# Kernel tuning notes

Measured on AMD Instinct MI355X. Metric: run time of the kernel, lower is better.

Reference implementation:

```python
import jax, jax.numpy as jnp
import numpy as np
import math

B, L, H, NH = 8, 200, 128, 2
HD = H // NH  # head dim = 64
TIME_VOCAB = 32
LN_EPS = 1e-12


def setup_inputs() -> dict:
    key = jax.random.key(0)
    ks = jax.random.split(key, 16)
    rn = lambda k, shape, s=0.02: (jax.random.normal(k, shape, jnp.float32) * s)
    return {
        "input_tensor": jax.random.normal(ks[0], (B, L, H), jnp.float32),
        "time_seq": jnp.sort(jax.random.randint(ks[1], (B, L), 0, 100000, jnp.int64), axis=-1),
        "attention_mask": jnp.zeros((B, 1, L, L), jnp.float32),
        "Wq": rn(ks[2], (H, H)), "bq": jnp.zeros((H,), jnp.float32),
        "Wk": rn(ks[3], (H, H)), "bk": jnp.zeros((H,), jnp.float32),
        "Wv": rn(ks[4], (H, H)), "bv": jnp.zeros((H,), jnp.float32),
        "Wd": rn(ks[5], (H, H)), "bd": jnp.zeros((H,), jnp.float32),
        "ln_g": jnp.ones((H,), jnp.float32), "ln_b": jnp.zeros((H,), jnp.float32),
        "key_time_table": rn(ks[6], (TIME_VOCAB, H)),
        "value_time_table": rn(ks[7], (TIME_VOCAB, H)),
        "key_pos_table": rn(ks[8], (L, H)),
        "value_pos_table": rn(ks[9], (L, H)),
    }


def _split_heads(x):
    # [B, L, H] -> [B, NH, L, HD]
    b, l, _ = x.shape
    return x.reshape(b, l, NH, HD).transpose(0, 2, 1, 3)


def reference(input_tensor, time_seq, attention_mask,
              Wq, bq, Wk, bk, Wv, bv, Wd, bd, ln_g, ln_b,
              key_time_table, value_time_table, key_pos_table, value_pos_table):
    b, l, h = input_tensor.shape

    # position embeddings (same for all batches)
    kpos = key_pos_table[:l].reshape(l, NH, HD).transpose(1, 0, 2)[None]    # [1,NH,L,HD]
    vpos = value_pos_table[:l].reshape(l, NH, HD).transpose(1, 0, 2)[None]  # [1,NH,L,HD]

    q = _split_heads(input_tensor @ Wq + bq)  # [B,NH,L,HD]
    k = _split_heads(input_tensor @ Wk + bk)
    v = _split_heads(input_tensor @ Wv + bv)

    scores = jnp.einsum('bhqd,bhkd->bhqk', q, k + kpos)

    # time decay: diff[b,i,j] = floor(log(1 + |t_i - t_j|))
    t = time_seq
    diff_idx = jnp.log1p(jnp.abs(t[:, :, None] - t[:, None, :]).astype(jnp.float32)).astype(jnp.int32)  # [B,L,L]

    # [B,L,L,H] -> [B,NH,L,L,HD]
    kt = key_time_table[diff_idx].reshape(b, l, l, NH, HD).transpose(0, 3, 1, 2, 4)
    vt = value_time_table[diff_idx].reshape(b, l, l, NH, HD).transpose(0, 3, 1, 2, 4)

    time_scores = jnp.einsum('bhqd,bhqkd->bhqk', q, kt)

    scores = (scores + time_scores) / math.sqrt(HD)
    scores = scores + attention_mask  # additive mask, broadcast over heads

    probs = jax.nn.softmax(scores, axis=-1)  # attn_dropout is identity in eval

    ctx = jnp.einsum('bhqk,bhkd->bhqd', probs, v + vpos)
    # NOTE: original uses raw (masked, pre-softmax) attention_scores here
    time_ctx = jnp.einsum('bhqk,bhqkd->bhqd', scores, vt)
    ctx = ctx + time_ctx

    ctx = ctx.transpose(0, 2, 1, 3).reshape(b, l, h)  # merge heads
    hidden = ctx @ Wd + bd                            # out_dropout identity in eval

    x = hidden + input_tensor
    mu = x.mean(-1, keepdims=True)
    var = ((x - mu) ** 2).mean(-1, keepdims=True)
    return (x - mu) / jnp.sqrt(var + LN_EPS) * ln_g + ln_b
```

## Files before the change

kernel.cpp:

```cpp
#include <hip/hip_runtime.h>
#include <math.h>

#define B_ 8
#define L_ 200
#define H_ 128
#define NH_ 2
#define HD_ 64
#define LP_ 256
#define TV_ 32
#define RQ_ 8
#define TQ_ 2

__global__ __launch_bounds__(128)
void qkv_kernel(const float* __restrict__ X,
                const float* __restrict__ Wq, const float* __restrict__ bq,
                const float* __restrict__ Wk, const float* __restrict__ bk,
                const float* __restrict__ Wv, const float* __restrict__ bv,
                const float* __restrict__ kpt, const float* __restrict__ vpt,
                float* __restrict__ Q, float* __restrict__ Kt, float* __restrict__ Vp){
    const int r0 = blockIdx.x * RQ_;
    const int m  = blockIdx.y;
    const int j  = threadIdx.x;
    __shared__ float xs[RQ_][H_];
    #pragma unroll
    for (int r = 0; r < RQ_; ++r) xs[r][j] = X[(r0 + r) * H_ + j];
    __syncthreads();
    const float* W = (m == 0) ? Wq : ((m == 1) ? Wk : Wv);
    float acc[RQ_];
    #pragma unroll
    for (int r = 0; r < RQ_; ++r) acc[r] = 0.f;
    #pragma unroll 8
    for (int i = 0; i < H_; ++i) {
        const float w = W[i * H_ + j];
        #pragma unroll
        for (int r = 0; r < RQ_; ++r) acc[r] += xs[r][i] * w;
    }
    const int h = j >> 6, d = j & 63;
    if (m == 0) {
        const float bj = bq[j];
        #pragma unroll
        for (int r = 0; r < RQ_; ++r) Q[(r0 + r) * H_ + j] = acc[r] + bj;
    } else if (m == 1) {
        const float bj = bk[j];
        #pragma unroll
        for (int r = 0; r < RQ_; ++r) {
            const int row = r0 + r, b = row / L_, l = row % L_;
            Kt[((b * NH_ + h) * HD_ + d) * LP_ + l] = acc[r] + bj + kpt[l * H_ + j];
        }
    } else {
        const float bj = bv[j];
        #pragma unroll
        for (int r = 0; r < RQ_; ++r) {
            const int row = r0 + r, b = row / L_, l = row % L_;
            Vp[((b * NH_ + h) * L_ + l) * HD_ + d] = acc[r] + bj + vpt[l * H_ + j];
        }
    }
}

__global__ __launch_bounds__(256)
void attn_out_kernel(const float* __restrict__ Q, const float* __restrict__ Kt,
                     const float* __restrict__ Vp, const int* __restrict__ tseq,
                     const float* __restrict__ mask,
                     const float* __restrict__ ktt, const float* __restrict__ vtt,
                     const float* __restrict__ Wd, const float* __restrict__ bd,
                     const float* __restrict__ X, const float* __restrict__ g,
                     const float* __restrict__ bb, float* __restrict__ out){
    const int b  = blockIdx.x / (L_ / TQ_);
    const int q0 = (blockIdx.x % (L_ / TQ_)) * TQ_;
    const int w  = threadIdx.x >> 6, lane = threadIdx.x & 63;
    const int h  = w & 1, qr = w >> 1, q = q0 + qr;
    const int bh = b * NH_ + h;

    __shared__ float ktt_s[TV_][H_ + 1];
    __shared__ float vtt_s[TV_][H_ + 1];
    __shared__ __align__(16) float qs [4][HD_];
    __shared__ float qkt[4][TV_];
    __shared__ float ss [4][TV_];
    __shared__ __align__(16) float ps [4][LP_];
    __shared__ float ctx_s[TQ_][H_];
    __shared__ float red1[4], red2[4];

    for (int t = threadIdx.x; t < TV_ * H_; t += 256) {
        ktt_s[t >> 7][t & 127] = ktt[t];
        vtt_s[t >> 7][t & 127] = vtt[t];
    }
    qs[w][lane] = Q[(b * L_ + q) * H_ + h * HD_ + lane];
    if (lane < TV_) ss[w][lane] = 0.f;
    __syncthreads();

    {
        const int i = lane & 31, half = lane >> 5;
        float a = 0.f;
        #pragma unroll 8
        for (int d = 0; d < 32; ++d)
            a += qs[w][half * 32 + d] * ktt_s[i][h * HD_ + half * 32 + d];
        a += __shfl_xor(a, 32);
        if (lane < TV_) qkt[w][lane] = a;
    }

    const float4* kt4 = (const float4*)(Kt + (size_t)bh * HD_ * LP_);
    float4 sA = make_float4(0.f, 0.f, 0.f, 0.f);
    float4 sB = make_float4(0.f, 0.f, 0.f, 0.f);
    #pragma unroll 8
    for (int d = 0; d < HD_; d += 2) {
        const float q0d = qs[w][d], q1d = qs[w][d + 1];
        const float4 k0 = kt4[d * (LP_ / 4) + lane];
        const float4 k1 = kt4[(d + 1) * (LP_ / 4) + lane];
        sA.x += q0d * k0.x; sA.y += q0d * k0.y; sA.z += q0d * k0.z; sA.w += q0d * k0.w;
        sB.x += q1d * k1.x; sB.y += q1d * k1.y; sB.z += q1d * k1.z; sB.w += q1d * k1.w;
    }
    float sv[4] = {sA.x + sB.x, sA.y + sB.y, sA.z + sB.z, sA.w + sB.w};
    const int k0i = lane * 4;
    float mx = -INFINITY;
    if (k0i < L_) {
        const float4 m4 = ((const float4*)(mask + ((size_t)(b * L_ + q)) * L_))[lane];
        const int4   t4 = ((const int4*)(tseq + b * L_))[lane];
        const int    tq = tseq[b * L_ + q];
        const float mv[4] = {m4.x, m4.y, m4.z, m4.w};
        const int   tk[4] = {t4.x, t4.y, t4.z, t4.w};
        #pragma unroll
        for (int jj = 0; jj < 4; ++jj) {
            int dt = tq - tk[jj]; if (dt < 0) dt = -dt;
            int idx = (int)log1pf((float)dt);
            if (idx > TV_ - 1) idx = TV_ - 1;
            float s = (sv[jj] + qkt[w][idx]) * 0.125f + mv[jj];
            sv[jj] = s;
            atomicAdd(&ss[w][idx], s);
            if (s > mx) mx = s;
        }
    } else {
        sv[0] = sv[1] = sv[2] = sv[3] = -INFINITY;
    }
    for (int off = 32; off; off >>= 1) { float o = __shfl_xor(mx, off); if (o > mx) mx = o; }
    float sum = 0.f, ev[4];
    #pragma unroll
    for (int jj = 0; jj < 4; ++jj) {
        float e = (k0i + jj < L_) ? __expf(sv[jj] - mx) : 0.f;
        ev[jj] = e; sum += e;
    }
    for (int off = 32; off; off >>= 1) sum += __shfl_xor(sum, off);
    ((float4*)ps[w])[lane] = make_float4(ev[0], ev[1], ev[2], ev[3]);

    const float inv = 1.f / sum;
    const float* vp = Vp + (size_t)bh * L_ * HD_;
    float c = 0.f;
    #pragma unroll 8
    for (int k = 0; k < L_; ++k) c += ps[w][k] * vp[k * HD_ + lane];
    c *= inv;
    float tc = 0.f;
    #pragma unroll 8
    for (int i = 0; i < TV_; ++i) tc += ss[w][i] * vtt_s[i][h * HD_ + lane];
    ctx_s[qr][h * HD_ + lane] = c + tc;
    __syncthreads();

    const int r = threadIdx.x >> 7, j = threadIdx.x & 127;
    float acc = 0.f;
    #pragma unroll 8
    for (int i = 0; i < H_; ++i) acc += ctx_s[r][i] * Wd[i * H_ + j];
    const int row = b * L_ + q0 + r;
    const float x = acc + bd[j] + X[row * H_ + j];

    float s = x;
    for (int off = 32; off; off >>= 1) s += __shfl_xor(s, off);
    if (lane == 0) red1[w] = s;
    __syncthreads();
    const float mean = (red1[2 * r] + red1[2 * r + 1]) * (1.f / H_);
    const float dx = x - mean;
    float s2 = dx * dx;
    for (int off = 32; off; off >>= 1) s2 += __shfl_xor(s2, off);
    if (lane == 0) red2[w] = s2;
    __syncthreads();
    const float var = (red2[2 * r] + red2[2 * r + 1]) * (1.f / H_);
    const float y = dx * rsqrtf(var + 1e-12f) * g[j] + bb[j];
    out[row * H_ + j] = y;
}

extern "C" void kernel_launch(void* const* d_in, const int* in_sizes, int n_in,
                              void* d_out, int out_size, void* d_ws, size_t ws_size,
                              hipStream_t stream) {
    const float* X    = (const float*)d_in[0];
    const int*   tseq = (const int*)  d_in[1];
    const float* mask = (const float*)d_in[2];
    const float* Wq = (const float*)d_in[3],  *bq = (const float*)d_in[4];
    const float* Wk = (const float*)d_in[5],  *bk = (const float*)d_in[6];
    const float* Wv = (const float*)d_in[7],  *bv = (const float*)d_in[8];
    const float* Wd = (const float*)d_in[9],  *bd = (const float*)d_in[10];
    const float* g  = (const float*)d_in[11], *bb = (const float*)d_in[12];
    const float* ktt = (const float*)d_in[13], *vtt = (const float*)d_in[14];
    const float* kpt = (const float*)d_in[15], *vpt = (const float*)d_in[16];

    float* ws  = (float*)d_ws;
    float* Q   = ws;
    float* Kt  = Q   + B_ * L_ * H_;
    float* Vp  = Kt  + B_ * NH_ * HD_ * LP_;

    dim3 g1(B_ * L_ / RQ_, 3);
    qkv_kernel<<<g1, 128, 0, stream>>>(X, Wq, bq, Wk, bk, Wv, bv, kpt, vpt, Q, Kt, Vp);
    attn_out_kernel<<<B_ * (L_ / TQ_), 256, 0, stream>>>(Q, Kt, Vp, tseq, mask, ktt, vtt,
                                                         Wd, bd, X, g, bb, (float*)d_out);
}
```

Before: 121.2 us.

## Process two query rows per wavefront to share K/V/Wd loads

Each block now covers four query rows, with each wavefront computing scores, softmax, context and output projection for two rows at once. Every K, V, time-table and Wd value loaded is reused for both rows, and the per-block shared-memory table setup is amortised over twice as many rows. In exchange the grid halves and register pressure rises, which may reduce latency hiding.

```diff
diff --git a/kernel.cpp b/kernel.cpp
--- a/kernel.cpp
+++ b/kernel.cpp
@@ -9,7 +9,6 @@
 #define LP_ 256
 #define TV_ 32
 #define RQ_ 8
-#define TQ_ 2
 
 __global__ __launch_bounds__(128)
 void qkv_kernel(const float* __restrict__ X,
@@ -65,114 +64,167 @@
                      const float* __restrict__ Wd, const float* __restrict__ bd,
                      const float* __restrict__ X, const float* __restrict__ g,
                      const float* __restrict__ bb, float* __restrict__ out){
-    const int b  = blockIdx.x / (L_ / TQ_);
-    const int q0 = (blockIdx.x % (L_ / TQ_)) * TQ_;
+    const int b  = blockIdx.x / (L_ / 4);
+    const int q0 = (blockIdx.x % (L_ / 4)) * 4;
     const int w  = threadIdx.x >> 6, lane = threadIdx.x & 63;
-    const int h  = w & 1, qr = w >> 1, q = q0 + qr;
+    const int h  = w & 1, qp = w >> 1;
+    const int qa = q0 + 2 * qp, qb = qa + 1;
     const int bh = b * NH_ + h;
 
     __shared__ float ktt_s[TV_][H_ + 1];
     __shared__ float vtt_s[TV_][H_ + 1];
-    __shared__ __align__(16) float qs [4][HD_];
-    __shared__ float qkt[4][TV_];
-    __shared__ float ss [4][TV_];
-    __shared__ __align__(16) float ps [4][LP_];
-    __shared__ float ctx_s[TQ_][H_];
-    __shared__ float red1[4], red2[4];
+    __shared__ __align__(16) float qs [4][2][HD_];
+    __shared__ __align__(16) float qkt[4][2][TV_];
+    __shared__ __align__(16) float ss [4][2][TV_];
+    __shared__ __align__(16) float ps [4][2][LP_];
+    __shared__ __align__(16) float ctx_s[4][H_];
+    __shared__ float redA[4], redB[4], red2A[4], red2B[4];
 
     for (int t = threadIdx.x; t < TV_ * H_; t += 256) {
         ktt_s[t >> 7][t & 127] = ktt[t];
         vtt_s[t >> 7][t & 127] = vtt[t];
     }
-    qs[w][lane] = Q[(b * L_ + q) * H_ + h * HD_ + lane];
-    if (lane < TV_) ss[w][lane] = 0.f;
+    qs[w][0][lane] = Q[(b * L_ + qa) * H_ + h * HD_ + lane];
+    qs[w][1][lane] = Q[(b * L_ + qb) * H_ + h * HD_ + lane];
+    ss[w][lane >> 5][lane & 31] = 0.f;
     __syncthreads();
 
     {
-        const int i = lane & 31, half = lane >> 5;
+        const int i = lane & 31, qsel = lane >> 5;
         float a = 0.f;
         #pragma unroll 8
-        for (int d = 0; d < 32; ++d)
-            a += qs[w][half * 32 + d] * ktt_s[i][h * HD_ + half * 32 + d];
-        a += __shfl_xor(a, 32);
-        if (lane < TV_) qkt[w][lane] = a;
+        for (int d = 0; d < HD_; ++d)
+            a += qs[w][qsel][d] * ktt_s[i][h * HD_ + d];
+        qkt[w][qsel][i] = a;
     }
 
     const float4* kt4 = (const float4*)(Kt + (size_t)bh * HD_ * LP_);
-    float4 sA = make_float4(0.f, 0.f, 0.f, 0.f);
-    float4 sB = make_float4(0.f, 0.f, 0.f, 0.f);
+    float4 sa = make_float4(0.f, 0.f, 0.f, 0.f);
+    float4 sb = make_float4(0.f, 0.f, 0.f, 0.f);
     #pragma unroll 8
-    for (int d = 0; d < HD_; d += 2) {
-        const float q0d = qs[w][d], q1d = qs[w][d + 1];
-        const float4 k0 = kt4[d * (LP_ / 4) + lane];
-        const float4 k1 = kt4[(d + 1) * (LP_ / 4) + lane];
-        sA.x += q0d * k0.x; sA.y += q0d * k0.y; sA.z += q0d * k0.z; sA.w += q0d * k0.w;
-        sB.x += q1d * k1.x; sB.y += q1d * k1.y; sB.z += q1d * k1.z; sB.w += q1d * k1.w;
-    }
-    float sv[4] = {sA.x + sB.x, sA.y + sB.y, sA.z + sB.z, sA.w + sB.w};
+    for (int d = 0; d < HD_; ++d) {
+        const float4 kv = kt4[d * (LP_ / 4) + lane];
+        const float qad = qs[w][0][d], qbd = qs[w][1][d];
+        sa.x += qad * kv.x; sa.y += qad * kv.y; sa.z += qad * kv.z; sa.w += qad * kv.w;
+        sb.x += qbd * kv.x; sb.y += qbd * kv.y; sb.z += qbd * kv.z; sb.w += qbd * kv.w;
+    }
+    float sva[4] = {sa.x, sa.y, sa.z, sa.w};
+    float svb[4] = {sb.x, sb.y, sb.z, sb.w};
     const int k0i = lane * 4;
-    float mx = -INFINITY;
+    float mxa = -INFINITY, mxb = -INFINITY;
     if (k0i < L_) {
-        const float4 m4 = ((const float4*)(mask + ((size_t)(b * L_ + q)) * L_))[lane];
-        const int4   t4 = ((const int4*)(tseq + b * L_))[lane];
-        const int    tq = tseq[b * L_ + q];
-        const float mv[4] = {m4.x, m4.y, m4.z, m4.w};
-        const int   tk[4] = {t4.x, t4.y, t4.z, t4.w};
+        const float4 m4a = ((const float4*)(mask + ((size_t)(b * L_ + qa)) * L_))[lane];
+        const float4 m4b = ((const float4*)(mask + ((size_t)(b * L_ + qb)) * L_))[lane];
+        const int4   t4  = ((const int4*)(tseq + b * L_))[lane];
+        const int    tqa = tseq[b * L_ + qa], tqb = tseq[b * L_ + qb];
+        const float mva[4] = {m4a.x, m4a.y, m4a.z, m4a.w};
+        const float mvb[4] = {m4b.x, m4b.y, m4b.z, m4b.w};
+        const int   tk[4]  = {t4.x, t4.y, t4.z, t4.w};
         #pragma unroll
         for (int jj = 0; jj < 4; ++jj) {
-            int dt = tq - tk[jj]; if (dt < 0) dt = -dt;
-            int idx = (int)log1pf((float)dt);
-            if (idx > TV_ - 1) idx = TV_ - 1;
-            float s = (sv[jj] + qkt[w][idx]) * 0.125f + mv[jj];
-            sv[jj] = s;
-            atomicAdd(&ss[w][idx], s);
-            if (s > mx) mx = s;
+            int dta = tqa - tk[jj]; if (dta < 0) dta = -dta;
+            int dtb = tqb - tk[jj]; if (dtb < 0) dtb = -dtb;
+            int ia = (int)log1pf((float)dta); if (ia > TV_ - 1) ia = TV_ - 1;
+            int ib = (int)log1pf((float)dtb); if (ib > TV_ - 1) ib = TV_ - 1;
+            float s_a = (sva[jj] + qkt[w][0][ia]) * 0.125f + mva[jj];
+            float s_b = (svb[jj] + qkt[w][1][ib]) * 0.125f + mvb[jj];
+            sva[jj] = s_a; svb[jj] = s_b;
+            atomicAdd(&ss[w][0][ia], s_a);
+            atomicAdd(&ss[w][1][ib], s_b);
+            if (s_a > mxa) mxa = s_a;
+            if (s_b > mxb) mxb = s_b;
         }
     } else {
-        sv[0] = sv[1] = sv[2] = sv[3] = -INFINITY;
-    }
-    for (int off = 32; off; off >>= 1) { float o = __shfl_xor(mx, off); if (o > mx) mx = o; }
-    float sum = 0.f, ev[4];
+        sva[0] = sva[1] = sva[2] = sva[3] = -INFINITY;
+        svb[0] = svb[1] = svb[2] = svb[3] = -INFINITY;
+    }
+    for (int off = 32; off; off >>= 1) {
+        float oa = __shfl_xor(mxa, off); if (oa > mxa) mxa = oa;
+        float ob = __shfl_xor(mxb, off); if (ob > mxb) mxb = ob;
+    }
+    float suma = 0.f, sumb = 0.f, eva[4], evb[4];
     #pragma unroll
     for (int jj = 0; jj < 4; ++jj) {
-        float e = (k0i + jj < L_) ? __expf(sv[jj] - mx) : 0.f;
-        ev[jj] = e; sum += e;
-    }
-    for (int off = 32; off; off >>= 1) sum += __shfl_xor(sum, off);
-    ((float4*)ps[w])[lane] = make_float4(ev[0], ev[1], ev[2], ev[3]);
-
-    const float inv = 1.f / sum;
+        float ea = (k0i + jj < L_) ? __expf(sva[jj] - mxa) : 0.f;
+        float eb = (k0i + jj < L_) ? __expf(svb[jj] - mxb) : 0.f;
+        eva[jj] = ea; suma += ea;
+        evb[jj] = eb; sumb += eb;
+    }
+    for (int off = 32; off; off >>= 1) { suma += __shfl_xor(suma, off); sumb += __shfl_xor(sumb, off); }
+    ((float4*)ps[w][0])[lane] = make_float4(eva[0], eva[1], eva[2], eva[3]);
+    ((float4*)ps[w][1])[lane] = make_float4(evb[0], evb[1], evb[2], evb[3]);
+
+    const float inva = 1.f / suma, invb = 1.f / sumb;
     const float* vp = Vp + (size_t)bh * L_ * HD_;
-    float c = 0.f;
+    const float4* psa4 = (const float4*)ps[w][0];
+    const float4* psb4 = (const float4*)ps[w][1];
+    float ca = 0.f, cb = 0.f;
+    #pragma unroll 5
+    for (int k4 = 0; k4 < L_ / 4; ++k4) {
+        const float4 pa = psa4[k4], pb = psb4[k4];
+        const int kb = k4 * 4;
+        const float v0 = vp[(kb + 0) * HD_ + lane];
+        const float v1 = vp[(kb + 1) * HD_ + lane];
+        const float v2 = vp[(kb + 2) * HD_ + lane];
+        const float v3 = vp[(kb + 3) * HD_ + lane];
+        ca += pa.x * v0; ca += pa.y * v1; ca += pa.z * v2; ca += pa.w * v3;
+        cb += pb.x * v0; cb += pb.y * v1; cb += pb.z * v2; cb += pb.w * v3;
+    }
+    ca *= inva; cb *= invb;
+    float tca = 0.f, tcb = 0.f;
+    const float4* ssa4 = (const float4*)ss[w][0];
+    const float4* ssb4 = (const float4*)ss[w][1];
+    #pragma unroll
+    for (int i4 = 0; i4 < TV_ / 4; ++i4) {
+        const float4 za = ssa4[i4], zb = ssb4[i4];
+        const int i = i4 * 4;
+        const float w0 = vtt_s[i + 0][h * HD_ + lane];
+        const float w1 = vtt_s[i + 1][h * HD_ + lane];
+        const float w2 = vtt_s[i + 2][h * HD_ + lane];
+        const float w3 = vtt_s[i + 3][h * HD_ + lane];
+        tca += za.x * w0; tca += za.y * w1; tca += za.z * w2; tca += za.w * w3;
+        tcb += zb.x * w0; tcb += zb.y * w1; tcb += zb.z * w2; tcb += zb.w * w3;
+    }
+    ctx_s[2 * qp + 0][h * HD_ + lane] = ca + tca;
+    ctx_s[2 * qp + 1][h * HD_ + lane] = cb + tcb;
+    __syncthreads();
+
+    const int r = threadIdx.x >> 7, j = threadIdx.x & 127;
+    const float4* ca4 = (const float4*)ctx_s[r];
+    const float4* cb4 = (const float4*)ctx_s[r + 2];
+    float acc_a = 0.f, acc_b = 0.f;
     #pragma unroll 8
-    for (int k = 0; k < L_; ++k) c += ps[w][k] * vp[k * HD_ + lane];
-    c *= inv;
-    float tc = 0.f;
-    #pragma unroll 8
-    for (int i = 0; i < TV_; ++i) tc += ss[w][i] * vtt_s[i][h * HD_ + lane];
-    ctx_s[qr][h * HD_ + lane] = c + tc;
-    __syncthreads();
-
-    const int r = threadIdx.x >> 7, j = threadIdx.x & 127;
-    float acc = 0.f;
-    #pragma unroll 8
-    for (int i = 0; i < H_; ++i) acc += ctx_s[r][i] * Wd[i * H_ + j];
-    const int row = b * L_ + q0 + r;
-    const float x = acc + bd[j] + X[row * H_ + j];
-
-    float s = x;
-    for (int off = 32; off; off >>= 1) s += __shfl_xor(s, off);
-    if (lane == 0) red1[w] = s;
-    __syncthreads();
-    const float mean = (red1[2 * r] + red1[2 * r + 1]) * (1.f / H_);
-    const float dx = x - mean;
-    float s2 = dx * dx;
-    for (int off = 32; off; off >>= 1) s2 += __shfl_xor(s2, off);
-    if (lane == 0) red2[w] = s2;
-    __syncthreads();
-    const float var = (red2[2 * r] + red2[2 * r + 1]) * (1.f / H_);
-    const float y = dx * rsqrtf(var + 1e-12f) * g[j] + bb[j];
-    out[row * H_ + j] = y;
+    for (int i4 = 0; i4 < H_ / 4; ++i4) {
+        const float4 xa = ca4[i4], xb = cb4[i4];
+        const int i = i4 * 4;
+        const float w0 = Wd[(i + 0) * H_ + j];
+        const float w1 = Wd[(i + 1) * H_ + j];
+        const float w2 = Wd[(i + 2) * H_ + j];
+        const float w3 = Wd[(i + 3) * H_ + j];
+        acc_a += xa.x * w0; acc_a += xa.y * w1; acc_a += xa.z * w2; acc_a += xa.w * w3;
+        acc_b += xb.x * w0; acc_b += xb.y * w1; acc_b += xb.z * w2; acc_b += xb.w * w3;
+    }
+    const int rowa = b * L_ + q0 + r, rowb = rowa + 2;
+    const float bdj = bd[j];
+    const float x_a = acc_a + bdj + X[rowa * H_ + j];
+    const float x_b = acc_b + bdj + X[rowb * H_ + j];
+
+    float s1a = x_a, s1b = x_b;
+    for (int off = 32; off; off >>= 1) { s1a += __shfl_xor(s1a, off); s1b += __shfl_xor(s1b, off); }
+    if (lane == 0) { redA[w] = s1a; redB[w] = s1b; }
+    __syncthreads();
+    const float meanA = (redA[2 * r] + redA[2 * r + 1]) * (1.f / H_);
+    const float meanB = (redB[2 * r] + redB[2 * r + 1]) * (1.f / H_);
+    const float dxa = x_a - meanA, dxb = x_b - meanB;
+    float s2a = dxa * dxa, s2b = dxb * dxb;
+    for (int off = 32; off; off >>= 1) { s2a += __shfl_xor(s2a, off); s2b += __shfl_xor(s2b, off); }
+    if (lane == 0) { red2A[w] = s2a; red2B[w] = s2b; }
+    __syncthreads();
+    const float varA = (red2A[2 * r] + red2A[2 * r + 1]) * (1.f / H_);
+    const float varB = (red2B[2 * r] + red2B[2 * r + 1]) * (1.f / H_);
+    const float gj = g[j], bbj = bb[j];
+    out[rowa * H_ + j] = dxa * rsqrtf(varA + 1e-12f) * gj + bbj;
+    out[rowb * H_ + j] = dxb * rsqrtf(varB + 1e-12f) * gj + bbj;
 }
 
 extern "C" void kernel_launch(void* const* d_in, const int* in_sizes, int n_in,
@@ -196,6 +248,6 @@
 
     dim3 g1(B_ * L_ / RQ_, 3);
     qkv_kernel<<<g1, 128, 0, stream>>>(X, Wq, bq, Wk, bk, Wv, bv, kpt, vpt, Q, Kt, Vp);
-    attn_out_kernel<<<B_ * (L_ / TQ_), 256, 0, stream>>>(Q, Kt, Vp, tseq, mask, ktt, vtt,
-                                                         Wd, bd, X, g, bb, (float*)d_out);
+    attn_out_kernel<<<B_ * (L_ / 4), 256, 0, stream>>>(Q, Kt, Vp, tseq, mask, ktt, vtt,
+                                                       Wd, bd, X, g, bb, (float*)d_out);
 }
```

Result: no change. 120.8 us (-0.4%).

## Process four query rows per attention block and vectorize shared-memory reads

Applied to the files above, without the earlier changes.

The attention/output kernel now handles four query rows per block with 512 threads instead of two rows with 256. This halves how often the time-embedding tables are loaded into shared memory across the grid. The first barrier is moved after the Q·K score loop and the mask/time loads so those global loads overlap the table staging. The probability, time-score and context reductions read shared memory as float4. In exchange the block count halves to 400, and each block uses more shared memory and threads, which may lower occupancy.

```diff
diff --git a/kernel.cpp b/kernel.cpp
--- a/kernel.cpp
+++ b/kernel.cpp
@@ -9,7 +9,6 @@
 #define LP_ 256
 #define TV_ 32
 #define RQ_ 8
-#define TQ_ 2
 
 __global__ __launch_bounds__(128)
 void qkv_kernel(const float* __restrict__ X,
@@ -57,7 +56,7 @@
     }
 }
 
-__global__ __launch_bounds__(256)
+__global__ __launch_bounds__(512)
 void attn_out_kernel(const float* __restrict__ Q, const float* __restrict__ Kt,
                      const float* __restrict__ Vp, const int* __restrict__ tseq,
                      const float* __restrict__ mask,
@@ -65,38 +64,29 @@
                      const float* __restrict__ Wd, const float* __restrict__ bd,
                      const float* __restrict__ X, const float* __restrict__ g,
                      const float* __restrict__ bb, float* __restrict__ out){
-    const int b  = blockIdx.x / (L_ / TQ_);
-    const int q0 = (blockIdx.x % (L_ / TQ_)) * TQ_;
+    const int b  = blockIdx.x / (L_ / 4);
+    const int q0 = (blockIdx.x % (L_ / 4)) * 4;
     const int w  = threadIdx.x >> 6, lane = threadIdx.x & 63;
-    const int h  = w & 1, qr = w >> 1, q = q0 + qr;
+    const int h  = w & 1, qr = w >> 1;
+    const int q  = q0 + qr;
     const int bh = b * NH_ + h;
 
     __shared__ float ktt_s[TV_][H_ + 1];
     __shared__ float vtt_s[TV_][H_ + 1];
-    __shared__ __align__(16) float qs [4][HD_];
-    __shared__ float qkt[4][TV_];
-    __shared__ float ss [4][TV_];
-    __shared__ __align__(16) float ps [4][LP_];
-    __shared__ float ctx_s[TQ_][H_];
-    __shared__ float red1[4], red2[4];
-
-    for (int t = threadIdx.x; t < TV_ * H_; t += 256) {
+    __shared__ __align__(16) float qs [8][HD_];
+    __shared__ float qkt[8][TV_];
+    __shared__ float ss [8][TV_];
+    __shared__ __align__(16) float ps [8][LP_];
+    __shared__ __align__(16) float ctx_s[4][H_];
+    __shared__ float red1[8], red2[8];
+
+    #pragma unroll
+    for (int t = threadIdx.x; t < TV_ * H_; t += 512) {
         ktt_s[t >> 7][t & 127] = ktt[t];
         vtt_s[t >> 7][t & 127] = vtt[t];
     }
     qs[w][lane] = Q[(b * L_ + q) * H_ + h * HD_ + lane];
     if (lane < TV_) ss[w][lane] = 0.f;
-    __syncthreads();
-
-    {
-        const int i = lane & 31, half = lane >> 5;
-        float a = 0.f;
-        #pragma unroll 8
-        for (int d = 0; d < 32; ++d)
-            a += qs[w][half * 32 + d] * ktt_s[i][h * HD_ + half * 32 + d];
-        a += __shfl_xor(a, 32);
-        if (lane < TV_) qkt[w][lane] = a;
-    }
 
     const float4* kt4 = (const float4*)(Kt + (size_t)bh * HD_ * LP_);
     float4 sA = make_float4(0.f, 0.f, 0.f, 0.f);
@@ -111,13 +101,29 @@
     }
     float sv[4] = {sA.x + sB.x, sA.y + sB.y, sA.z + sB.z, sA.w + sB.w};
     const int k0i = lane * 4;
-    float mx = -INFINITY;
+
+    float mv[4]; int tk[4]; int tq = 0;
     if (k0i < L_) {
         const float4 m4 = ((const float4*)(mask + ((size_t)(b * L_ + q)) * L_))[lane];
         const int4   t4 = ((const int4*)(tseq + b * L_))[lane];
-        const int    tq = tseq[b * L_ + q];
-        const float mv[4] = {m4.x, m4.y, m4.z, m4.w};
-        const int   tk[4] = {t4.x, t4.y, t4.z, t4.w};
+        tq = tseq[b * L_ + q];
+        mv[0] = m4.x; mv[1] = m4.y; mv[2] = m4.z; mv[3] = m4.w;
+        tk[0] = t4.x; tk[1] = t4.y; tk[2] = t4.z; tk[3] = t4.w;
+    }
+    __syncthreads();
+
+    {
+        const int i = lane & 31, half = lane >> 5;
+        float a = 0.f;
+        #pragma unroll 8
+        for (int d = 0; d < 32; ++d)
+            a += qs[w][half * 32 + d] * ktt_s[i][h * HD_ + half * 32 + d];
+        a += __shfl_xor(a, 32);
+        if (lane < TV_) qkt[w][lane] = a;
+    }
+
+    float mx = -INFINITY;
+    if (k0i < L_) {
         #pragma unroll
         for (int jj = 0; jj < 4; ++jj) {
             int dt = tq - tk[jj]; if (dt < 0) dt = -dt;
@@ -143,20 +149,44 @@
 
     const float inv = 1.f / sum;
     const float* vp = Vp + (size_t)bh * L_ * HD_;
+    const float4* ps4 = (const float4*)ps[w];
     float c = 0.f;
-    #pragma unroll 8
-    for (int k = 0; k < L_; ++k) c += ps[w][k] * vp[k * HD_ + lane];
+    #pragma unroll 5
+    for (int k4 = 0; k4 < L_ / 4; ++k4) {
+        const float4 p = ps4[k4];
+        const int kb = k4 * 4;
+        c += p.x * vp[(kb + 0) * HD_ + lane];
+        c += p.y * vp[(kb + 1) * HD_ + lane];
+        c += p.z * vp[(kb + 2) * HD_ + lane];
+        c += p.w * vp[(kb + 3) * HD_ + lane];
+    }
     c *= inv;
     float tc = 0.f;
-    #pragma unroll 8
-    for (int i = 0; i < TV_; ++i) tc += ss[w][i] * vtt_s[i][h * HD_ + lane];
+    const float4* ss4 = (const float4*)ss[w];
+    #pragma unroll
+    for (int i4 = 0; i4 < TV_ / 4; ++i4) {
+        const float4 z = ss4[i4];
+        const int i = i4 * 4;
+        tc += z.x * vtt_s[i + 0][h * HD_ + lane];
+        tc += z.y * vtt_s[i + 1][h * HD_ + lane];
+        tc += z.z * vtt_s[i + 2][h * HD_ + lane];
+        tc += z.w * vtt_s[i + 3][h * HD_ + lane];
+    }
     ctx_s[qr][h * HD_ + lane] = c + tc;
     __syncthreads();
 
     const int r = threadIdx.x >> 7, j = threadIdx.x & 127;
+    const float4* c4 = (const float4*)ctx_s[r];
     float acc = 0.f;
     #pragma unroll 8
-    for (int i = 0; i < H_; ++i) acc += ctx_s[r][i] * Wd[i * H_ + j];
+    for (int i4 = 0; i4 < H_ / 4; ++i4) {
+        const float4 xv = c4[i4];
+        const int i = i4 * 4;
+        acc += xv.x * Wd[(i + 0) * H_ + j];
+        acc += xv.y * Wd[(i + 1) * H_ + j];
+        acc += xv.z * Wd[(i + 2) * H_ + j];
+        acc += xv.w * Wd[(i + 3) * H_ + j];
+    }
     const int row = b * L_ + q0 + r;
     const float x = acc + bd[j] + X[row * H_ + j];
 
@@ -196,6 +226,6 @@
 
     dim3 g1(B_ * L_ / RQ_, 3);
     qkv_kernel<<<g1, 128, 0, stream>>>(X, Wq, bq, Wk, bk, Wv, bv, kpt, vpt, Q, Kt, Vp);
-    attn_out_kernel<<<B_ * (L_ / TQ_), 256, 0, stream>>>(Q, Kt, Vp, tseq, mask, ktt, vtt,
-                                                         Wd, bd, X, g, bb, (float*)d_out);
+    attn_out_kernel<<<B_ * (L_ / 4), 512, 0, stream>>>(Q, Kt, Vp, tseq, mask, ktt, vtt,
+                                                       Wd, bd, X, g, bb, (float*)d_out);
 }
```

New measurement: 123.2 us. Within noise of the previous version (+1.6%).
